# Kernel optimization log

Hardware: AMD Instinct MI355X
Metric: run time of the kernel (lower is better)

## Reference

```python
import jax, jax.numpy as jnp
import numpy as np

N_NODES = 100000
N_EDGES = 1600000
IN_DIM = 128
HID = 32
HEADS = 4
OUT_DIM = 40
BN_EPS = 1e-5
NEG_SLOPE = 0.2


def _gat_conv(x, src, dst, W, att_src, att_dst, bias, concat):
    # x: [N, F_in]; src/dst: [E] (self-loops already appended)
    H, C = att_src.shape
    h = (x @ W).reshape(-1, H, C)                       # [N, H, C]
    a_s = jnp.sum(h * att_src, axis=-1)                 # [N, H]
    a_d = jnp.sum(h * att_dst, axis=-1)                 # [N, H]
    e = jax.nn.leaky_relu(a_s[src] + a_d[dst], NEG_SLOPE)  # [E, H]
    # segment softmax over incoming edges of each destination node
    m = jax.ops.segment_max(e, dst, num_segments=N_NODES)
    m = jnp.where(jnp.isfinite(m), m, 0.0)
    p = jnp.exp(e - m[dst])
    denom = jax.ops.segment_sum(p, dst, num_segments=N_NODES)
    alpha = p / (denom[dst] + 1e-16)                    # [E, H]
    out = jax.ops.segment_sum(h[src] * alpha[..., None], dst, num_segments=N_NODES)  # [N, H, C]
    out = out.reshape(N_NODES, H * C) if concat else out.mean(axis=1)
    return out + bias


def _bn_eval(x, gamma, beta, rm, rv):
    return (x - rm) * jax.lax.rsqrt(rv + BN_EPS) * gamma + beta


def setup_inputs() -> dict:
    key = jax.random.key(0)
    ks = jax.random.split(key, 16)
    d = {}
    d["x"] = jax.random.normal(ks[0], (N_NODES, IN_DIM), dtype=jnp.float32)
    d["edge_index"] = jax.random.randint(ks[1], (2, N_EDGES), 0, N_NODES, dtype=jnp.int64 if jax.config.jax_enable_x64 else jnp.int32)
    s = 0.1
    # conv1: IN_DIM -> HID x HEADS (concat)
    d["W1"] = jax.random.normal(ks[2], (IN_DIM, HEADS * HID), jnp.float32) * s
    d["as1"] = jax.random.normal(ks[3], (HEADS, HID), jnp.float32) * s
    d["ad1"] = jax.random.normal(ks[4], (HEADS, HID), jnp.float32) * s
    d["b1"] = jnp.zeros((HEADS * HID,), jnp.float32)
    d["g1"] = jnp.ones((HEADS * HID,), jnp.float32)
    d["beta1"] = jnp.zeros((HEADS * HID,), jnp.float32)
    d["rm1"] = jnp.zeros((HEADS * HID,), jnp.float32)
    d["rv1"] = jnp.ones((HEADS * HID,), jnp.float32)
    # conv2: HID*HEADS -> HID (1 head, no concat)
    d["W2"] = jax.random.normal(ks[5], (HEADS * HID, HID), jnp.float32) * s
    d["as2"] = jax.random.normal(ks[6], (1, HID), jnp.float32) * s
    d["ad2"] = jax.random.normal(ks[7], (1, HID), jnp.float32) * s
    d["b2"] = jnp.zeros((HID,), jnp.float32)
    d["g2"] = jnp.ones((HID,), jnp.float32)
    d["beta2"] = jnp.zeros((HID,), jnp.float32)
    d["rm2"] = jnp.zeros((HID,), jnp.float32)
    d["rv2"] = jnp.ones((HID,), jnp.float32)
    # conv3: HID -> OUT_DIM (1 head, no concat)
    d["W3"] = jax.random.normal(ks[8], (HID, OUT_DIM), jnp.float32) * s
    d["as3"] = jax.random.normal(ks[9], (1, OUT_DIM), jnp.float32) * s
    d["ad3"] = jax.random.normal(ks[10], (1, OUT_DIM), jnp.float32) * s
    d["b3"] = jnp.zeros((OUT_DIM,), jnp.float32)
    return d


def reference(x, edge_index, W1, as1, ad1, b1, g1, beta1, rm1, rv1,
              W2, as2, ad2, b2, g2, beta2, rm2, rv2, W3, as3, ad3, b3):
    # add self-loops (PyG GATConv default), shared by all three layers
    loops = jnp.arange(N_NODES, dtype=edge_index.dtype)
    src = jnp.concatenate([edge_index[0], loops])
    dst = jnp.concatenate([edge_index[1], loops])
    h = _gat_conv(x, src, dst, W1, as1, ad1, b1, concat=True)
    h = jax.nn.elu(_bn_eval(h, g1, beta1, rm1, rv1))
    h = _gat_conv(h, src, dst, W2, as2, ad2, b2, concat=False)
    h = jax.nn.elu(_bn_eval(h, g2, beta2, rm2, rv2))
    out = _gat_conv(h, src, dst, W3, as3, ad3, b3, concat=False)
    return jax.nn.log_softmax(out, axis=1)
```

## Files before the change

### kernel.cpp

```cpp
#include <hip/hip_runtime.h>
#include <math.h>

#define N_NODES 100000
#define N_EDGES 1600000
#define E_TOT   (N_EDGES + N_NODES)
#define BN_EPS  1e-5f
#define NEG_SLOPE 0.2f
#define NINF (-INFINITY)

__device__ __forceinline__ unsigned short f2bf(float f) {
    unsigned int u = __float_as_uint(f);
    unsigned int r = (u + 0x7FFFu + ((u >> 16) & 1u)) >> 16;
    return (unsigned short)r;
}
__device__ __forceinline__ float bflo(unsigned int v) {
    return __uint_as_float(v << 16);
}
__device__ __forceinline__ float bfhi(unsigned int v) {
    return __uint_as_float(v & 0xFFFF0000u);
}
__device__ __forceinline__ float sel4(float a, float b, float c, float d, int i) {
    float lo = (i & 1) ? b : a;
    float hi = (i & 1) ? d : c;
    return (i & 2) ? hi : lo;
}


__global__ __launch_bounds__(256) void k_count(const int* __restrict__ ei,
                                               int* __restrict__ cnt) {
    int i = blockIdx.x * blockDim.x + threadIdx.x;
    if (i >= E_TOT) return;
    int d = (i < N_EDGES) ? ei[N_EDGES + i] : (i - N_EDGES);
    atomicAdd(&cnt[d], 1);
}

__global__ __launch_bounds__(256) void k_scan1(const int* __restrict__ cnt,
                                               int* __restrict__ excl,
                                               int* __restrict__ sums) {
    __shared__ int lds[256];
    int t = threadIdx.x;
    int base = blockIdx.x * 1024 + t * 4;
    int a[4];
#pragma unroll
    for (int j = 0; j < 4; ++j) a[j] = (base + j < N_NODES) ? cnt[base + j] : 0;
    int tot = a[0] + a[1] + a[2] + a[3];
    lds[t] = tot;
    __syncthreads();
    for (int off = 1; off < 256; off <<= 1) {
        int v = (t >= off) ? lds[t - off] : 0;
        __syncthreads();
        lds[t] += v;
        __syncthreads();
    }
    int run = lds[t] - tot;
#pragma unroll
    for (int j = 0; j < 4; ++j) {
        if (base + j < N_NODES) excl[base + j] = run;
        run += a[j];
    }
    if (t == 255) sums[blockIdx.x] = lds[255];
}

__global__ void k_scan2(int* sums, int nb) {
    if (blockIdx.x == 0 && threadIdx.x == 0) {
        int run = 0;
        for (int i = 0; i < nb; ++i) { int v = sums[i]; sums[i] = run; run += v; }
    }
}

__global__ __launch_bounds__(256) void k_scan3(int* __restrict__ row_ptr,
                                               int* __restrict__ cursor,
                                               const int* __restrict__ sums) {
    int i = blockIdx.x * blockDim.x + threadIdx.x;
    if (i == 0) row_ptr[N_NODES] = E_TOT;
    if (i >= N_NODES) return;
    int v = row_ptr[i] + sums[i >> 10];
    row_ptr[i] = v;
    cursor[i] = v;
}

__global__ __launch_bounds__(256) void k_scatter(const int* __restrict__ ei,
                                                 int* __restrict__ cursor,
                                                 int* __restrict__ col_idx) {
    int i = blockIdx.x * blockDim.x + threadIdx.x;
    if (i >= E_TOT) return;
    int s, d;
    if (i < N_EDGES) { s = ei[i]; d = ei[N_EDGES + i]; }
    else             { s = d = i - N_EDGES; }
    int pos = atomicAdd(&cursor[d], 1);
    __builtin_nontemporal_store(s, &col_idx[pos]);
}


template <int K, int NC, int BM, int BLOCK>
__global__ __launch_bounds__(BLOCK) void k_gemm(const float* __restrict__ X,
                                                const float* __restrict__ W,
                                                float* __restrict__ Hout,
                                                int nrows) {
    constexpr int CG  = NC / 4;
    constexpr int TR  = BLOCK / CG;
    constexpr int RPT = BM / TR;
    constexpr int LDK = K + 4;
    __shared__ float xs[BM * LDK];
    const int row0 = blockIdx.x * BM;
    const int vr = (nrows - row0 < BM) ? (nrows - row0) : BM;
    const int nvalid = vr * K;
    for (int i = threadIdx.x * 4; i < BM * K; i += BLOCK * 4) {
        float4 v = make_float4(0.f, 0.f, 0.f, 0.f);
        if (i < nvalid) v = *(const float4*)(X + (size_t)row0 * K + i);
        int row = i / K, col = i % K;
        *(float4*)(&xs[row * LDK + col]) = v;
    }
    __syncthreads();
    const int tx = threadIdx.x % CG;
    const int ty = threadIdx.x / CG;
    float4 acc[RPT];
#pragma unroll
    for (int r = 0; r < RPT; ++r) acc[r] = make_float4(0.f, 0.f, 0.f, 0.f);
    for (int k4 = 0; k4 < K / 4; ++k4) {
        const float4 w0 = *(const float4*)(W + (k4 * 4 + 0) * NC + tx * 4);
        const float4 w1 = *(const float4*)(W + (k4 * 4 + 1) * NC + tx * 4);
        const float4 w2 = *(const float4*)(W + (k4 * 4 + 2) * NC + tx * 4);
        const float4 w3 = *(const float4*)(W + (k4 * 4 + 3) * NC + tx * 4);
#pragma unroll
        for (int r = 0; r < RPT; ++r) {
            const float4 xv = *(const float4*)(&xs[(ty * RPT + r) * LDK + k4 * 4]);
            acc[r].x = fmaf(xv.w, w3.x, fmaf(xv.z, w2.x, fmaf(xv.y, w1.x, fmaf(xv.x, w0.x, acc[r].x))));
            acc[r].y = fmaf(xv.w, w3.y, fmaf(xv.z, w2.y, fmaf(xv.y, w1.y, fmaf(xv.x, w0.y, acc[r].y))));
            acc[r].z = fmaf(xv.w, w3.z, fmaf(xv.z, w2.z, fmaf(xv.y, w1.z, fmaf(xv.x, w0.z, acc[r].z))));
            acc[r].w = fmaf(xv.w, w3.w, fmaf(xv.z, w2.w, fmaf(xv.y, w1.w, fmaf(xv.x, w0.w, acc[r].w))));
        }
    }
#pragma unroll
    for (int r = 0; r < RPT; ++r) {
        int row = row0 + ty * RPT + r;
        if (row < nrows) *(float4*)(Hout + (size_t)row * NC + tx * 4) = acc[r];
    }
}


template <int K, int NC, int BM, int BLOCK, int HEADS_, bool BF16OUT>
__global__ __launch_bounds__(BLOCK) void k_gemm_ap(const float* __restrict__ X,
                                                   const float* __restrict__ W,
                                                   const float* __restrict__ asf,
                                                   const float* __restrict__ adf,
                                                   float* __restrict__ a_s,
                                                   float* __restrict__ a_d,
                                                   void* __restrict__ Hout,
                                                   int nrows) {
    constexpr int CG  = NC / 4;
    constexpr int TR  = BLOCK / CG;
    constexpr int RPT = BM / TR;
    constexpr int LDK = K + 4;
    constexpr int GL  = NC / HEADS_ / 4;
    static_assert(GL == 8, "epilogue assumes 8-lane groups");
    __shared__ float xs[BM * LDK];
    const int row0 = blockIdx.x * BM;
    const int vr = (nrows - row0 < BM) ? (nrows - row0) : BM;
    const int nvalid = vr * K;
    for (int i = threadIdx.x * 4; i < BM * K; i += BLOCK * 4) {
        float4 v = make_float4(0.f, 0.f, 0.f, 0.f);
        if (i < nvalid) v = *(const float4*)(X + (size_t)row0 * K + i);
        int row = i / K, col = i % K;
        *(float4*)(&xs[row * LDK + col]) = v;
    }
    __syncthreads();
    const int tx = threadIdx.x % CG;
    const int ty = threadIdx.x / CG;
    float4 acc[RPT];
#pragma unroll
    for (int r = 0; r < RPT; ++r) acc[r] = make_float4(0.f, 0.f, 0.f, 0.f);
    for (int k4 = 0; k4 < K / 4; ++k4) {
        const float4 w0 = *(const float4*)(W + (k4 * 4 + 0) * NC + tx * 4);
        const float4 w1 = *(const float4*)(W + (k4 * 4 + 1) * NC + tx * 4);
        const float4 w2 = *(const float4*)(W + (k4 * 4 + 2) * NC + tx * 4);
        const float4 w3 = *(const float4*)(W + (k4 * 4 + 3) * NC + tx * 4);
#pragma unroll
        for (int r = 0; r < RPT; ++r) {
            const float4 xv = *(const float4*)(&xs[(ty * RPT + r) * LDK + k4 * 4]);
            acc[r].x = fmaf(xv.w, w3.x, fmaf(xv.z, w2.x, fmaf(xv.y, w1.x, fmaf(xv.x, w0.x, acc[r].x))));
            acc[r].y = fmaf(xv.w, w3.y, fmaf(xv.z, w2.y, fmaf(xv.y, w1.y, fmaf(xv.x, w0.y, acc[r].y))));
            acc[r].z = fmaf(xv.w, w3.z, fmaf(xv.z, w2.z, fmaf(xv.y, w1.z, fmaf(xv.x, w0.z, acc[r].z))));
            acc[r].w = fmaf(xv.w, w3.w, fmaf(xv.z, w2.w, fmaf(xv.y, w1.w, fmaf(xv.x, w0.w, acc[r].w))));
        }
    }
    const int head = tx >> 3;
    const float4 asv = *(const float4*)(asf + tx * 4);
    const float4 adv = *(const float4*)(adf + tx * 4);
#pragma unroll
    for (int r = 0; r < RPT; ++r) {
        int row = row0 + ty * RPT + r;
        float ps = acc[r].x * asv.x + acc[r].y * asv.y + acc[r].z * asv.z + acc[r].w * asv.w;
        float pd = acc[r].x * adv.x + acc[r].y * adv.y + acc[r].z * adv.z + acc[r].w * adv.w;
#pragma unroll
        for (int off = 1; off < GL; off <<= 1) {
            ps += __shfl_xor(ps, off);
            pd += __shfl_xor(pd, off);
        }
        if (row < nrows) {
            if constexpr (BF16OUT) {
                ushort4 o;
                o.x = f2bf(acc[r].x); o.y = f2bf(acc[r].y);
                o.z = f2bf(acc[r].z); o.w = f2bf(acc[r].w);
                *(ushort4*)((unsigned short*)Hout + (size_t)row * NC + tx * 4) = o;
            } else {
                *(float4*)((float*)Hout + (size_t)row * NC + tx * 4) = acc[r];
            }
            if ((tx & (GL - 1)) == 0) {
                a_s[(size_t)row * HEADS_ + head] = ps;
                a_d[(size_t)row * HEADS_ + head] = pd;
            }
        }
    }
}


__global__ __launch_bounds__(256) void k_attproj3(const float* __restrict__ h,
                                                  const float* __restrict__ asf,
                                                  const float* __restrict__ adf,
                                                  float* __restrict__ a_s,
                                                  float* __restrict__ a_d) {
    int wv = (blockIdx.x * blockDim.x + threadIdx.x) >> 6;
    int lane = threadIdx.x & 63;
    if (wv >= N_NODES) return;
    float hv = (lane < 40) ? h[(size_t)wv * 40 + lane] : 0.f;
    float s = (lane < 40) ? hv * asf[lane] : 0.f;
    float d = (lane < 40) ? hv * adf[lane] : 0.f;
#pragma unroll
    for (int off = 1; off < 64; off <<= 1) { s += __shfl_xor(s, off); d += __shfl_xor(d, off); }
    if (lane == 0) { a_s[wv] = s; a_d[wv] = d; }
}


__global__ __launch_bounds__(256) void k_agg1(const unsigned short* __restrict__ hb,
                                              const float* __restrict__ a_s,
                                              const float* __restrict__ a_d,
                                              const int* __restrict__ row_ptr,
                                              const int* __restrict__ col_idx,
                                              const float* __restrict__ b,
                                              const float* __restrict__ g,
                                              const float* __restrict__ beta,
                                              const float* __restrict__ rm,
                                              const float* __restrict__ rv,
                                              float* __restrict__ obuf) {
    __shared__ float4 lp[4 * 64];
    __shared__ int    lc[4 * 64];
    const int wid  = threadIdx.x >> 6;
    const int lane = threadIdx.x & 63;
    const int n = (blockIdx.x << 2) + wid;
    if (n >= N_NODES) return;
    float4* lpw = lp + (wid << 6);
    int*    lcw = lc + (wid << 6);
    const int hd = lane >> 4;
    const float4 ad4 = *(const float4*)(a_d + (size_t)n * 4);
    const int beg = row_ptr[n], end = row_ptr[n + 1];
    const int deg = end - beg;
    float den0 = 0.f, den1 = 0.f, den2 = 0.f, den3 = 0.f;
    float acc0 = 0.f, acc1 = 0.f;

    if (deg <= 64) {
        const int idx = beg + lane;
        const bool v = idx < end;
        const int col = v ? col_idx[idx] : 0;
        float e0, e1, e2, e3;
        if (v) {
            float4 as4 = *(const float4*)(a_s + (size_t)col * 4);
            e0 = as4.x + ad4.x; e0 = e0 > 0.f ? e0 : NEG_SLOPE * e0;
            e1 = as4.y + ad4.y; e1 = e1 > 0.f ? e1 : NEG_SLOPE * e1;
            e2 = as4.z + ad4.z; e2 = e2 > 0.f ? e2 : NEG_SLOPE * e2;
            e3 = as4.w + ad4.w; e3 = e3 > 0.f ? e3 : NEG_SLOPE * e3;
        } else { e0 = e1 = e2 = e3 = NINF; }
        float m0 = e0, m1 = e1, m2 = e2, m3 = e3;
#pragma unroll
        for (int off = 1; off < 64; off <<= 1) {
            m0 = fmaxf(m0, __shfl_xor(m0, off));
            m1 = fmaxf(m1, __shfl_xor(m1, off));
            m2 = fmaxf(m2, __shfl_xor(m2, off));
            m3 = fmaxf(m3, __shfl_xor(m3, off));
        }
        float p0 = __expf(e0 - m0), p1 = __expf(e1 - m1);
        float p2 = __expf(e2 - m2), p3 = __expf(e3 - m3);
        lpw[lane] = make_float4(p0, p1, p2, p3);
        lcw[lane] = col;
        den0 = p0; den1 = p1; den2 = p2; den3 = p3;
#pragma unroll
        for (int off = 1; off < 64; off <<= 1) {
            den0 += __shfl_xor(den0, off); den1 += __shfl_xor(den1, off);
            den2 += __shfl_xor(den2, off); den3 += __shfl_xor(den3, off);
        }
        const int cnt = (deg + 3) & ~3;
        for (int j = 0; j < cnt; j += 4) {
            float4 pa = lpw[j],     pb = lpw[j + 1];
            float4 pc = lpw[j + 2], pq = lpw[j + 3];
            int c0 = lcw[j], c1 = lcw[j + 1], c2 = lcw[j + 2], c3 = lcw[j + 3];
            unsigned int v0 = *(const unsigned int*)(hb + (size_t)c0 * 128 + 2 * lane);
            unsigned int v1 = *(const unsigned int*)(hb + (size_t)c1 * 128 + 2 * lane);
            unsigned int v2 = *(const unsigned int*)(hb + (size_t)c2 * 128 + 2 * lane);
            unsigned int v3 = *(const unsigned int*)(hb + (size_t)c3 * 128 + 2 * lane);
            float pA0 = sel4(pa.x, pa.y, pa.z, pa.w, hd);
            float pA1 = sel4(pb.x, pb.y, pb.z, pb.w, hd);
            float pA2 = sel4(pc.x, pc.y, pc.z, pc.w, hd);
            float pA3 = sel4(pq.x, pq.y, pq.z, pq.w, hd);
            acc0 += pA0 * bflo(v0) + pA1 * bflo(v1) + pA2 * bflo(v2) + pA3 * bflo(v3);
            acc1 += pA0 * bfhi(v0) + pA1 * bfhi(v1) + pA2 * bfhi(v2) + pA3 * bfhi(v3);
        }
    } else {
        float m0 = NINF, m1 = NINF, m2 = NINF, m3 = NINF;
        for (int c = beg; c < end; c += 64) {
            int idx = c + lane;
            bool v = idx < end;
            if (v) {
                int col = col_idx[idx];
                float4 as4 = *(const float4*)(a_s + (size_t)col * 4);
                float e0 = as4.x + ad4.x; e0 = e0 > 0.f ? e0 : NEG_SLOPE * e0;
                float e1 = as4.y + ad4.y; e1 = e1 > 0.f ? e1 : NEG_SLOPE * e1;
                float e2 = as4.z + ad4.z; e2 = e2 > 0.f ? e2 : NEG_SLOPE * e2;
                float e3 = as4.w + ad4.w; e3 = e3 > 0.f ? e3 : NEG_SLOPE * e3;
                m0 = fmaxf(m0, e0); m1 = fmaxf(m1, e1);
                m2 = fmaxf(m2, e2); m3 = fmaxf(m3, e3);
            }
        }
#pragma unroll
        for (int off = 1; off < 64; off <<= 1) {
            m0 = fmaxf(m0, __shfl_xor(m0, off));
            m1 = fmaxf(m1, __shfl_xor(m1, off));
            m2 = fmaxf(m2, __shfl_xor(m2, off));
            m3 = fmaxf(m3, __shfl_xor(m3, off));
        }
        for (int c = beg; c < end; c += 64) {
            int idx = c + lane;
            bool v = idx < end;
            int col = v ? col_idx[idx] : 0;
            float p0 = 0.f, p1 = 0.f, p2 = 0.f, p3 = 0.f;
            if (v) {
                float4 as4 = *(const float4*)(a_s + (size_t)col * 4);
                float e0 = as4.x + ad4.x; e0 = e0 > 0.f ? e0 : NEG_SLOPE * e0;
                float e1 = as4.y + ad4.y; e1 = e1 > 0.f ? e1 : NEG_SLOPE * e1;
                float e2 = as4.z + ad4.z; e2 = e2 > 0.f ? e2 : NEG_SLOPE * e2;
                float e3 = as4.w + ad4.w; e3 = e3 > 0.f ? e3 : NEG_SLOPE * e3;
                p0 = __expf(e0 - m0); p1 = __expf(e1 - m1);
                p2 = __expf(e2 - m2); p3 = __expf(e3 - m3);
            }
            lpw[lane] = make_float4(p0, p1, p2, p3);
            lcw[lane] = col;
            float s0 = p0, s1 = p1, s2 = p2, s3 = p3;
#pragma unroll
            for (int off = 1; off < 64; off <<= 1) {
                s0 += __shfl_xor(s0, off); s1 += __shfl_xor(s1, off);
                s2 += __shfl_xor(s2, off); s3 += __shfl_xor(s3, off);
            }
            den0 += s0; den1 += s1; den2 += s2; den3 += s3;
            int csz = end - c; if (csz > 64) csz = 64;
            int cnt = (csz + 3) & ~3;
            for (int j = 0; j < cnt; j += 4) {
                float4 pa = lpw[j],     pb = lpw[j + 1];
                float4 pc = lpw[j + 2], pq = lpw[j + 3];
                int c0i = lcw[j], c1i = lcw[j + 1], c2i = lcw[j + 2], c3i = lcw[j + 3];
                unsigned int v0 = *(const unsigned int*)(hb + (size_t)c0i * 128 + 2 * lane);
                unsigned int v1 = *(const unsigned int*)(hb + (size_t)c1i * 128 + 2 * lane);
                unsigned int v2 = *(const unsigned int*)(hb + (size_t)c2i * 128 + 2 * lane);
                unsigned int v3 = *(const unsigned int*)(hb + (size_t)c3i * 128 + 2 * lane);
                float pA0 = sel4(pa.x, pa.y, pa.z, pa.w, hd);
                float pA1 = sel4(pb.x, pb.y, pb.z, pb.w, hd);
                float pA2 = sel4(pc.x, pc.y, pc.z, pc.w, hd);
                float pA3 = sel4(pq.x, pq.y, pq.z, pq.w, hd);
                acc0 += pA0 * bflo(v0) + pA1 * bflo(v1) + pA2 * bflo(v2) + pA3 * bflo(v3);
                acc1 += pA0 * bfhi(v0) + pA1 * bfhi(v1) + pA2 * bfhi(v2) + pA3 * bfhi(v3);
            }
        }
    }

    float dsel = sel4(den0, den1, den2, den3, hd);
    float inv = 1.f / (dsel + 1e-16f);
    float f0 = acc0 * inv;
    float f1 = acc1 * inv;
    const int fA = lane * 2;
    float2 bb  = *(const float2*)(b + fA);
    float2 gg  = *(const float2*)(g + fA);
    float2 be  = *(const float2*)(beta + fA);
    float2 rmm = *(const float2*)(rm + fA);
    float2 rvv = *(const float2*)(rv + fA);
    f0 = (f0 + bb.x - rmm.x) * rsqrtf(rvv.x + BN_EPS) * gg.x + be.x;
    f1 = (f1 + bb.y - rmm.y) * rsqrtf(rvv.y + BN_EPS) * gg.y + be.y;
    f0 = f0 > 0.f ? f0 : (__expf(f0) - 1.f);
    f1 = f1 > 0.f ? f1 : (__expf(f1) - 1.f);
    *(float2*)(obuf + (size_t)n * 128 + fA) = make_float2(f0, f1);
}

__global__ __launch_bounds__(256) void k_agg2(const float* __restrict__ h,
                                              const float* __restrict__ a_s,
                                              const float* __restrict__ a_d,
                                              const int* __restrict__ row_ptr,
                                              const int* __restrict__ col_idx,
                                              const float* __restrict__ b,
                                              const float* __restrict__ g,
                                              const float* __restrict__ beta,
                                              const float* __restrict__ rm,
                                              const float* __restrict__ rv,
                                              float* __restrict__ obuf) {
    __shared__ float lp[4 * 64];
    __shared__ int   lc[4 * 64];
    const int wid  = threadIdx.x >> 6;
    const int lane = threadIdx.x & 63;
    const int n = (blockIdx.x << 2) + wid;
    if (n >= N_NODES) return;
    float* lpw = lp + (wid << 6);
    int*   lcw = lc + (wid << 6);
    const int l31 = lane & 31, hh = lane >> 5;
    const float ad = a_d[n];
    const int beg = row_ptr[n], end = row_ptr[n + 1];
    const int deg = end - beg;
    float den = 0.f, acc = 0.f;

    if (deg <= 64) {
        const int idx = beg + lane;
        const bool v = idx < end;
        const int col = v ? col_idx[idx] : 0;
        float e = NINF;
        if (v) {
            e = a_s[col] + ad;
            e = e > 0.f ? e : NEG_SLOPE * e;
        }
        float m = e;
#pragma unroll
        for (int off = 1; off < 64; off <<= 1) m = fmaxf(m, __shfl_xor(m, off));
        float p = __expf(e - m);
        lpw[lane] = p;
        lcw[lane] = col;
        den = p;
#pragma unroll
        for (int off = 1; off < 64; off <<= 1) den += __shfl_xor(den, off);
        const int cnt = (deg + 7) & ~7;
        for (int j = 0; j < cnt; j += 8) {
            int j0 = j + (hh << 2);
            float p0 = lpw[j0], p1 = lpw[j0 + 1], p2 = lpw[j0 + 2], p3 = lpw[j0 + 3];
            int c0 = lcw[j0], c1 = lcw[j0 + 1], c2 = lcw[j0 + 2], c3 = lcw[j0 + 3];
            acc += p0 * h[(size_t)c0 * 32 + l31] + p1 * h[(size_t)c1 * 32 + l31]
                 + p2 * h[(size_t)c2 * 32 + l31] + p3 * h[(size_t)c3 * 32 + l31];
        }
    } else {
        float m = NINF;
        for (int c = beg; c < end; c += 64) {
            int idx = c + lane;
            if (idx < end) {
                float e = a_s[col_idx[idx]] + ad;
                e = e > 0.f ? e : NEG_SLOPE * e;
                m = fmaxf(m, e);
            }
        }
#pragma unroll
        for (int off = 1; off < 64; off <<= 1) m = fmaxf(m, __shfl_xor(m, off));
        for (int c = beg; c < end; c += 64) {
            int idx = c + lane;
            bool v = idx < end;
            int col = v ? col_idx[idx] : 0;
            float p = 0.f;
            if (v) {
                float e = a_s[col] + ad;
                e = e > 0.f ? e : NEG_SLOPE * e;
                p = __expf(e - m);
            }
            lpw[lane] = p;
            lcw[lane] = col;
            float s = p;
#pragma unroll
            for (int off = 1; off < 64; off <<= 1) s += __shfl_xor(s, off);
            den += s;
            int csz = end - c; if (csz > 64) csz = 64;
            int cnt = (csz + 7) & ~7;
            for (int j = 0; j < cnt; j += 8) {
                int j0 = j + (hh << 2);
                float p0 = lpw[j0], p1 = lpw[j0 + 1], p2 = lpw[j0 + 2], p3 = lpw[j0 + 3];
                int c0 = lcw[j0], c1 = lcw[j0 + 1], c2 = lcw[j0 + 2], c3 = lcw[j0 + 3];
                acc += p0 * h[(size_t)c0 * 32 + l31] + p1 * h[(size_t)c1 * 32 + l31]
                     + p2 * h[(size_t)c2 * 32 + l31] + p3 * h[(size_t)c3 * 32 + l31];
            }
        }
    }
    acc += __shfl_xor(acc, 32);
    float vout = acc / (den + 1e-16f);
    vout += b[l31];
    vout = (vout - rm[l31]) * rsqrtf(rv[l31] + BN_EPS) * g[l31] + beta[l31];
    vout = vout > 0.f ? vout : (__expf(vout) - 1.f);
    if (lane < 32) obuf[(size_t)n * 32 + lane] = vout;
}

__global__ __launch_bounds__(256) void k_agg3(const float* __restrict__ h,
                                              const float* __restrict__ a_s,
                                              const float* __restrict__ a_d,
                                              const int* __restrict__ row_ptr,
                                              const int* __restrict__ col_idx,
                                              const float* __restrict__ b,
                                              float* __restrict__ out) {
    __shared__ float lp[4 * 64];
    __shared__ int   lc[4 * 64];
    const int wid  = threadIdx.x >> 6;
    const int lane = threadIdx.x & 63;
    const int n = (blockIdx.x << 2) + wid;
    if (n >= N_NODES) return;
    float* lpw = lp + (wid << 6);
    int*   lcw = lc + (wid << 6);
    const float ad = a_d[n];
    const int beg = row_ptr[n], end = row_ptr[n + 1];
    const int deg = end - beg;
    float den = 0.f, acc = 0.f;

    if (deg <= 64) {
        const int idx = beg + lane;
        const bool v = idx < end;
        const int col = v ? col_idx[idx] : 0;
        float e = NINF;
        if (v) {
            e = a_s[col] + ad;
            e = e > 0.f ? e : NEG_SLOPE * e;
        }
        float m = e;
#pragma unroll
        for (int off = 1; off < 64; off <<= 1) m = fmaxf(m, __shfl_xor(m, off));
        float p = __expf(e - m);
        lpw[lane] = p;
        lcw[lane] = col;
        den = p;
#pragma unroll
        for (int off = 1; off < 64; off <<= 1) den += __shfl_xor(den, off);
        const int cnt = (deg + 3) & ~3;
        for (int j = 0; j < cnt; j += 4) {
            float p0 = lpw[j], p1 = lpw[j + 1], p2 = lpw[j + 2], p3 = lpw[j + 3];
            int c0 = lcw[j], c1 = lcw[j + 1], c2 = lcw[j + 2], c3 = lcw[j + 3];
            if (lane < 40) {
                acc += p0 * h[(size_t)c0 * 40 + lane] + p1 * h[(size_t)c1 * 40 + lane]
                     + p2 * h[(size_t)c2 * 40 + lane] + p3 * h[(size_t)c3 * 40 + lane];
            }
        }
    } else {
        float m = NINF;
        for (int c = beg; c < end; c += 64) {
            int idx = c + lane;
            if (idx < end) {
                float e = a_s[col_idx[idx]] + ad;
                e = e > 0.f ? e : NEG_SLOPE * e;
                m = fmaxf(m, e);
            }
        }
#pragma unroll
        for (int off = 1; off < 64; off <<= 1) m = fmaxf(m, __shfl_xor(m, off));
        for (int c = beg; c < end; c += 64) {
            int idx = c + lane;
            bool v = idx < end;
            int col = v ? col_idx[idx] : 0;
            float p = 0.f;
            if (v) {
                float e = a_s[col] + ad;
                e = e > 0.f ? e : NEG_SLOPE * e;
                p = __expf(e - m);
            }
            lpw[lane] = p;
            lcw[lane] = col;
            float s = p;
#pragma unroll
            for (int off = 1; off < 64; off <<= 1) s += __shfl_xor(s, off);
            den += s;
            int csz = end - c; if (csz > 64) csz = 64;
            int cnt = (csz + 3) & ~3;
            for (int j = 0; j < cnt; j += 4) {
                float p0 = lpw[j], p1 = lpw[j + 1], p2 = lpw[j + 2], p3 = lpw[j + 3];
                int c0 = lcw[j], c1 = lcw[j + 1], c2 = lcw[j + 2], c3 = lcw[j + 3];
                if (lane < 40) {
                    acc += p0 * h[(size_t)c0 * 40 + lane] + p1 * h[(size_t)c1 * 40 + lane]
                         + p2 * h[(size_t)c2 * 40 + lane] + p3 * h[(size_t)c3 * 40 + lane];
                }
            }
        }
    }
    float vv = acc / (den + 1e-16f) + b[lane < 40 ? lane : 0];
    float vm = (lane < 40) ? vv : NINF;
#pragma unroll
    for (int off = 1; off < 64; off <<= 1) vm = fmaxf(vm, __shfl_xor(vm, off));
    float ex = (lane < 40) ? __expf(vv - vm) : 0.f;
#pragma unroll
    for (int off = 1; off < 64; off <<= 1) ex += __shfl_xor(ex, off);
    float res = vv - vm - logf(ex);
    if (lane < 40) out[(size_t)n * 40 + lane] = res;
}


extern "C" void kernel_launch(void* const* d_in, const int* in_sizes, int n_in,
                              void* d_out, int out_size, void* d_ws, size_t ws_size,
                              hipStream_t stream) {
    const float* x    = (const float*)d_in[0];
    const int*   ei   = (const int*)d_in[1];
    const float* W1   = (const float*)d_in[2];
    const float* as1  = (const float*)d_in[3];
    const float* ad1  = (const float*)d_in[4];
    const float* b1   = (const float*)d_in[5];
    const float* g1   = (const float*)d_in[6];
    const float* be1  = (const float*)d_in[7];
    const float* rm1  = (const float*)d_in[8];
    const float* rv1  = (const float*)d_in[9];
    const float* W2   = (const float*)d_in[10];
    const float* as2  = (const float*)d_in[11];
    const float* ad2  = (const float*)d_in[12];
    const float* b2   = (const float*)d_in[13];
    const float* g2   = (const float*)d_in[14];
    const float* be2  = (const float*)d_in[15];
    const float* rm2  = (const float*)d_in[16];
    const float* rv2  = (const float*)d_in[17];
    const float* W3   = (const float*)d_in[18];
    const float* as3  = (const float*)d_in[19];
    const float* ad3  = (const float*)d_in[20];
    const float* b3   = (const float*)d_in[21];
    float* out = (float*)d_out;

    char* base = (char*)d_ws;
    size_t off = 0;
    auto carve = [&](size_t bytes) {
        char* p = base + off;
        off = (off + bytes + 255) & ~(size_t)255;
        return p;
    };
    int*   row_ptr = (int*)carve((N_NODES + 1) * sizeof(int));
    int*   cnt     = (int*)carve(N_NODES * sizeof(int));
    int*   cursor  = (int*)carve(N_NODES * sizeof(int));
    int*   sums    = (int*)carve(1024 * sizeof(int));
    int*   col_idx = (int*)carve((size_t)E_TOT * sizeof(int));
    float* a_s     = (float*)carve((size_t)N_NODES * 4 * sizeof(float));
    float* a_d     = (float*)carve((size_t)N_NODES * 4 * sizeof(float));
    float* hbuf    = (float*)carve((size_t)N_NODES * 128 * sizeof(float));
    float* obuf    = (float*)carve((size_t)N_NODES * 128 * sizeof(float));
    (void)ws_size;

    hipMemsetAsync(cnt, 0, N_NODES * sizeof(int), stream);
    {
        int g1b = (E_TOT + 255) / 256;
        k_count<<<g1b, 256, 0, stream>>>(ei, cnt);
        int nb = (N_NODES + 1023) / 1024;
        k_scan1<<<nb, 256, 0, stream>>>(cnt, row_ptr, sums);
        k_scan2<<<1, 1, 0, stream>>>(sums, nb);
        k_scan3<<<(N_NODES + 255) / 256, 256, 0, stream>>>(row_ptr, cursor, sums);
        k_scatter<<<g1b, 256, 0, stream>>>(ei, cursor, col_idx);
    }

    const int GEMM_GRID = (N_NODES + 63) / 64;
    const int WPN = (N_NODES + 3) / 4;

    k_gemm_ap<128, 128, 64, 256, 4, true><<<GEMM_GRID, 256, 0, stream>>>(
        x, W1, as1, ad1, a_s, a_d, (void*)hbuf, N_NODES);
    k_agg1<<<WPN, 256, 0, stream>>>((const unsigned short*)hbuf, a_s, a_d,
                                    row_ptr, col_idx,
                                    b1, g1, be1, rm1, rv1, obuf);

    k_gemm_ap<128, 32, 64, 256, 1, false><<<GEMM_GRID, 256, 0, stream>>>(
        obuf, W2, as2, ad2, a_s, a_d, (void*)hbuf, N_NODES);
    k_agg2<<<WPN, 256, 0, stream>>>(hbuf, a_s, a_d, row_ptr, col_idx,
                                    b2, g2, be2, rm2, rv2, obuf);

    k_gemm<32, 40, 64, 320><<<GEMM_GRID, 320, 0, stream>>>(obuf, W3, hbuf, N_NODES);
    k_attproj3<<<WPN, 256, 0, stream>>>(hbuf, as3, ad3, a_s, a_d);
    k_agg3<<<WPN, 256, 0, stream>>>(hbuf, a_s, a_d, row_ptr, col_idx, b3, out);
}
```

Before: 664.8 us.

## Build CSR via two-level bucketed scatter to localize atomics and writes

Measured after the change: 635.8 us. 1.05x faster.

```diff
diff --git a/kernel.cpp b/kernel.cpp
--- a/kernel.cpp
+++ b/kernel.cpp
@@ -7,6 +7,10 @@
 #define BN_EPS  1e-5f
 #define NEG_SLOPE 0.2f
 #define NINF (-INFINITY)
+
+#define NPB   2048
+#define NBUCK ((N_NODES + NPB - 1) / NPB)
+#define EPB   4096
 
 __device__ __forceinline__ unsigned short f2bf(float f) {
     unsigned int u = __float_as_uint(f);
@@ -69,26 +73,117 @@
 }
 
 __global__ __launch_bounds__(256) void k_scan3(int* __restrict__ row_ptr,
-                                               int* __restrict__ cursor,
                                                const int* __restrict__ sums) {
     int i = blockIdx.x * blockDim.x + threadIdx.x;
     if (i == 0) row_ptr[N_NODES] = E_TOT;
     if (i >= N_NODES) return;
-    int v = row_ptr[i] + sums[i >> 10];
-    row_ptr[i] = v;
-    cursor[i] = v;
-}
-
-__global__ __launch_bounds__(256) void k_scatter(const int* __restrict__ ei,
-                                                 int* __restrict__ cursor,
-                                                 int* __restrict__ col_idx) {
-    int i = blockIdx.x * blockDim.x + threadIdx.x;
-    if (i >= E_TOT) return;
-    int s, d;
-    if (i < N_EDGES) { s = ei[i]; d = ei[N_EDGES + i]; }
-    else             { s = d = i - N_EDGES; }
-    int pos = atomicAdd(&cursor[d], 1);
-    __builtin_nontemporal_store(s, &col_idx[pos]);
+    row_ptr[i] += sums[i >> 10];
+}
+
+
+__global__ __launch_bounds__(256) void kb_hist(const int* __restrict__ ei,
+                                               int* __restrict__ bucket_cnt) {
+    __shared__ int h[NBUCK];
+    for (int t = threadIdx.x; t < NBUCK; t += 256) h[t] = 0;
+    __syncthreads();
+    const int base = blockIdx.x * EPB;
+#pragma unroll
+    for (int j = 0; j < EPB / 256; ++j) {
+        int i = base + j * 256 + threadIdx.x;
+        if (i < E_TOT) {
+            int d = (i < N_EDGES) ? ei[N_EDGES + i] : (i - N_EDGES);
+            atomicAdd(&h[d >> 11], 1);
+        }
+    }
+    __syncthreads();
+    for (int t = threadIdx.x; t < NBUCK; t += 256)
+        if (h[t]) atomicAdd(&bucket_cnt[t], h[t]);
+}
+
+__global__ void kb_scan(const int* __restrict__ bucket_cnt,
+                        int* __restrict__ bucket_base,
+                        int* __restrict__ bucket_cursor) {
+    if (blockIdx.x == 0 && threadIdx.x == 0) {
+        int run = 0;
+        for (int b = 0; b < NBUCK; ++b) {
+            bucket_base[b] = run;
+            bucket_cursor[b] = run;
+            run += bucket_cnt[b];
+        }
+        bucket_base[NBUCK] = run;
+    }
+}
+
+__global__ __launch_bounds__(256) void kb_stage(const int* __restrict__ ei,
+                                                int* __restrict__ bucket_cursor,
+                                                unsigned int* __restrict__ estage) {
+    __shared__ int h[NBUCK], base_l[NBUCK], cnt2[NBUCK], gbase[NBUCK];
+    __shared__ unsigned int recs[EPB];
+    for (int t = threadIdx.x; t < NBUCK; t += 256) { h[t] = 0; cnt2[t] = 0; }
+    __syncthreads();
+    const int base = blockIdx.x * EPB;
+    int myb[EPB / 256];
+    unsigned int myrec[EPB / 256];
+#pragma unroll
+    for (int j = 0; j < EPB / 256; ++j) {
+        int i = base + j * 256 + threadIdx.x;
+        myb[j] = -1;
+        myrec[j] = 0;
+        if (i < E_TOT) {
+            int s, d;
+            if (i < N_EDGES) { s = ei[i]; d = ei[N_EDGES + i]; }
+            else             { s = d = i - N_EDGES; }
+            int b = d >> 11;
+            myb[j] = b;
+            myrec[j] = ((unsigned int)(d & (NPB - 1)) << 17) | (unsigned int)s;
+            atomicAdd(&h[b], 1);
+        }
+    }
+    __syncthreads();
+    if (threadIdx.x == 0) {
+        int run = 0;
+        for (int b = 0; b < NBUCK; ++b) { base_l[b] = run; run += h[b]; }
+    }
+    __syncthreads();
+    for (int t = threadIdx.x; t < NBUCK; t += 256)
+        gbase[t] = h[t] ? atomicAdd(&bucket_cursor[t], h[t]) : 0;
+#pragma unroll
+    for (int j = 0; j < EPB / 256; ++j) {
+        if (myb[j] >= 0) {
+            int pos = base_l[myb[j]] + atomicAdd(&cnt2[myb[j]], 1);
+            recs[pos] = myrec[j];
+        }
+    }
+    __syncthreads();
+    int m = E_TOT - base; if (m > EPB) m = EPB;
+    for (int i = threadIdx.x; i < m; i += 256) {
+        int lo = 0, hi = NBUCK - 1;
+        while (lo < hi) {
+            int mid = (lo + hi + 1) >> 1;
+            if (base_l[mid] <= i) lo = mid; else hi = mid - 1;
+        }
+        estage[gbase[lo] + (i - base_l[lo])] = recs[i];
+    }
+}
+
+__global__ __launch_bounds__(256) void kb_scatter(const unsigned int* __restrict__ estage,
+                                                  const int* __restrict__ bucket_base,
+                                                  const int* __restrict__ row_ptr,
+                                                  int* __restrict__ col_idx) {
+    __shared__ int cur[NPB];
+    const int b = blockIdx.x;
+    const int n0 = b * NPB;
+    int nn = N_NODES - n0; if (nn > NPB) nn = NPB;
+    for (int i = threadIdx.x; i < nn; i += 256) cur[i] = row_ptr[n0 + i];
+    __syncthreads();
+    const int e1 = bucket_base[b + 1];
+    for (int i = bucket_base[b] + threadIdx.x; i < e1; i += 256) {
+        unsigned int r = estage[i];
+        int dl = (int)(r >> 17);
+        int s  = (int)(r & 0x1FFFFu);
+        int pos = atomicAdd(&cur[dl], 1);
+        col_idx[pos] = s;
+    }
 }
 
 
@@ -618,26 +713,34 @@
         off = (off + bytes + 255) & ~(size_t)255;
         return p;
     };
-    int*   row_ptr = (int*)carve((N_NODES + 1) * sizeof(int));
-    int*   cnt     = (int*)carve(N_NODES * sizeof(int));
-    int*   cursor  = (int*)carve(N_NODES * sizeof(int));
-    int*   sums    = (int*)carve(1024 * sizeof(int));
-    int*   col_idx = (int*)carve((size_t)E_TOT * sizeof(int));
-    float* a_s     = (float*)carve((size_t)N_NODES * 4 * sizeof(float));
-    float* a_d     = (float*)carve((size_t)N_NODES * 4 * sizeof(float));
-    float* hbuf    = (float*)carve((size_t)N_NODES * 128 * sizeof(float));
-    float* obuf    = (float*)carve((size_t)N_NODES * 128 * sizeof(float));
+    int*   row_ptr  = (int*)carve((N_NODES + 1) * sizeof(int));
+    int*   cnt      = (int*)carve(N_NODES * sizeof(int));
+    int*   sums     = (int*)carve(1024 * sizeof(int));
+    int*   bucket_cnt    = (int*)carve((NBUCK + 1) * sizeof(int));
+    int*   bucket_base   = (int*)carve((NBUCK + 1) * sizeof(int));
+    int*   bucket_cursor = (int*)carve((NBUCK + 1) * sizeof(int));
+    int*   col_idx  = (int*)carve((size_t)E_TOT * sizeof(int));
+    unsigned int* estage = (unsigned int*)carve((size_t)E_TOT * sizeof(unsigned int));
+    float* a_s      = (float*)carve((size_t)N_NODES * 4 * sizeof(float));
+    float* a_d      = (float*)carve((size_t)N_NODES * 4 * sizeof(float));
+    float* hbuf     = (float*)carve((size_t)N_NODES * 128 * sizeof(float));
+    float* obuf     = (float*)carve((size_t)N_NODES * 128 * sizeof(float));
     (void)ws_size;
 
     hipMemsetAsync(cnt, 0, N_NODES * sizeof(int), stream);
+    hipMemsetAsync(bucket_cnt, 0, (NBUCK + 1) * sizeof(int), stream);
     {
         int g1b = (E_TOT + 255) / 256;
         k_count<<<g1b, 256, 0, stream>>>(ei, cnt);
         int nb = (N_NODES + 1023) / 1024;
         k_scan1<<<nb, 256, 0, stream>>>(cnt, row_ptr, sums);
         k_scan2<<<1, 1, 0, stream>>>(sums, nb);
-        k_scan3<<<(N_NODES + 255) / 256, 256, 0, stream>>>(row_ptr, cursor, sums);
-        k_scatter<<<g1b, 256, 0, stream>>>(ei, cursor, col_idx);
+        k_scan3<<<(N_NODES + 255) / 256, 256, 0, stream>>>(row_ptr, sums);
+        int gsb = (E_TOT + EPB - 1) / EPB;
+        kb_hist<<<gsb, 256, 0, stream>>>(ei, bucket_cnt);
+        kb_scan<<<1, 1, 0, stream>>>(bucket_cnt, bucket_base, bucket_cursor);
+        kb_stage<<<gsb, 256, 0, stream>>>(ei, bucket_cursor, estage);
+        kb_scatter<<<NBUCK, 256, 0, stream>>>(estage, bucket_base, row_ptr, col_idx);
     }
 
     const int GEMM_GRID = (N_NODES + 63) / 64;
```
